# Kernel optimization log

Measured on AMD Instinct MI355X. Metric: run time of the kernel, lower is better.

Reference implementation:

```python
import jax, jax.numpy as jnp
import numpy as np

EMBED = 1024
D_MODEL = 1024
HEADS = 16
HEAD_DIM = D_MODEL // HEADS


def setup_inputs() -> dict:
    key = jax.random.key(0)
    ks = jax.random.split(key, 9)
    s = 1.0 / np.sqrt(EMBED)
    inp = {
        "x": jax.random.normal(ks[0], (4, 2048, EMBED), dtype=jnp.float32),
        "Wq": jax.random.uniform(ks[1], (EMBED, D_MODEL), jnp.float32, -s, s),
        "bq": jax.random.uniform(ks[2], (D_MODEL,), jnp.float32, -s, s),
        "Wk": jax.random.uniform(ks[3], (EMBED, D_MODEL), jnp.float32, -s, s),
        "bk": jax.random.uniform(ks[4], (D_MODEL,), jnp.float32, -s, s),
        "Wv": jax.random.uniform(ks[5], (EMBED, D_MODEL), jnp.float32, -s, s),
        "bv": jax.random.uniform(ks[6], (D_MODEL,), jnp.float32, -s, s),
        "Wo": jax.random.uniform(ks[7], (D_MODEL, D_MODEL), jnp.float32, -s, s),
        "bo": jax.random.uniform(ks[8], (D_MODEL,), jnp.float32, -s, s),
    }
    return inp


def reference(x, Wq, bq, Wk, bk, Wv, bv, Wo, bo):
    B, S, _ = x.shape
    # projections -> [B, H, S, Dh]
    def proj(W, b):
        return (x @ W + b).reshape(B, S, HEADS, HEAD_DIM).transpose(0, 2, 1, 3)
    q = proj(Wq, bq)
    k = proj(Wk, bk)
    v = proj(Wv, bv)
    energy = jnp.einsum("bhqd,bhkd->bhqk", q, k)  # [B,H,S,S]
    attn = jax.nn.softmax(energy / jnp.sqrt(jnp.float32(HEAD_DIM)), axis=-1)
    out = jnp.einsum("bhqk,bhkd->bhqd", attn, v)
    out = out.transpose(0, 2, 1, 3).reshape(B, S, D_MODEL)
    return out @ Wo + bo
```

## Files before the change

### kernel.cpp

```cpp
#include <hip/hip_runtime.h>

typedef unsigned short u16;
typedef unsigned int u32;
typedef unsigned short u16x8 __attribute__((ext_vector_type(8)));
typedef unsigned int u32x4 __attribute__((ext_vector_type(4)));
typedef __bf16 bf16x8 __attribute__((ext_vector_type(8)));
typedef float f32x4 __attribute__((ext_vector_type(4)));

#define QSCALE 0.18033688011112042f

__device__ __forceinline__ u16 f2bf(float f) {
    unsigned u = __float_as_uint(f);
    u += 0x7fffu + ((u >> 16) & 1u);
    return (u16)(u >> 16);
}

__device__ __forceinline__ u32 cvtpk(float lo, float hi) {
    u32 r;
    asm("v_cvt_pk_bf16_f32 %0, %1, %2" : "=v"(r) : "v"(lo), "v"(hi));
    return r;
}

__device__ __forceinline__ bf16x8 ldfrag(const u16* p) {
    return __builtin_bit_cast(bf16x8, *(const u16x8*)p);
}

__device__ __forceinline__ void async_cp16(const void* g, void* l) {
    __builtin_amdgcn_global_load_lds(
        (const __attribute__((address_space(1))) unsigned int*)g,
        (__attribute__((address_space(3))) unsigned int*)l, 16, 0, 0);
}

__device__ __forceinline__ uint2 pack4(float a, float b, float c, float d) {
    uint2 w;
    w.x = (u32)f2bf(a) | ((u32)f2bf(b) << 16);
    w.y = (u32)f2bf(c) | ((u32)f2bf(d) << 16);
    return w;
}

__device__ __forceinline__ f32x4 mfma32(bf16x8 a, bf16x8 b, f32x4 c) {
    return __builtin_amdgcn_mfma_f32_16x16x32_bf16(a, b, c, 0, 0, 0);
}


__global__ void cvt_x(const float* __restrict__ x, u16* __restrict__ xb, int n4) {
    int i = blockIdx.x * blockDim.x + threadIdx.x;
    if (i < n4) {
        float4 v = ((const float4*)x)[i];
        ushort4 o;
        o.x = f2bf(v.x); o.y = f2bf(v.y); o.z = f2bf(v.z); o.w = f2bf(v.w);
        ((ushort4*)xb)[i] = o;
    }
}

__global__ __launch_bounds__(1024) void transp(const float* __restrict__ src, u16* __restrict__ dst) {
    __shared__ float t[32][33];
    int bx = blockIdx.x * 32, by = blockIdx.y * 32;
    t[threadIdx.y][threadIdx.x] = src[(by + threadIdx.y) * 1024 + bx + threadIdx.x];
    __syncthreads();
    dst[(bx + threadIdx.y) * 1024 + by + threadIdx.x] = f2bf(t[threadIdx.x][threadIdx.y]);
}

__global__ void mkbias(const float* __restrict__ bq, const float* __restrict__ bk,
                       const float* __restrict__ bv, float* __restrict__ bqkv) {
    int i = blockIdx.x * blockDim.x + threadIdx.x;
    if (i < 3072) bqkv[i] = (i < 1024) ? bq[i] : (i < 2048 ? bk[i - 1024] : bv[i - 2048]);
}


template <int EPI>
__global__ __launch_bounds__(512)
void gemm256(const u16* __restrict__ A, const u16* __restrict__ Bt,
             const float* __restrict__ bias,
             u16* __restrict__ Qb, u16* __restrict__ Kb, u16* __restrict__ Vt,
             float* __restrict__ outf) {
    __shared__ u16 Asm3[3][256 * 64];
    __shared__ u16 Bsm3[3][128 * 64];

    int tid = threadIdx.x;
    int wave = tid >> 6, lane = tid & 63;
    int lr = lane & 15, lq = lane >> 4;
    int wrow = (wave >> 1) * 64, wcol = (wave & 1) * 64;
    int tileM = blockIdx.y * 256, tileN = blockIdx.x * 128;

    f32x4 acc[4][4];
#pragma unroll
    for (int i = 0; i < 4; i++)
#pragma unroll
        for (int j = 0; j < 4; j++)
            acc[i][j] = (f32x4){0.f, 0.f, 0.f, 0.f};

    int srow = tid >> 3;
    int sgrp = (tid & 7) ^ (srow & 7);
    const u16* gA = A + (tileM + srow) * 1024 + sgrp * 8;
    const u16* gB = Bt + (tileN + srow) * 1024 + sgrp * 8;

#define STAGE(buf, kc)                                                        \
    do {                                                                      \
        _Pragma("unroll")                                                     \
        for (int r = 0; r < 4; ++r)                                           \
            async_cp16(gA + (kc) + r * 64 * 1024, &Asm3[buf][tid * 8 + r * 4096]); \
        _Pragma("unroll")                                                     \
        for (int r = 0; r < 2; ++r)                                           \
            async_cp16(gB + (kc) + r * 64 * 1024, &Bsm3[buf][tid * 8 + r * 4096]); \
    } while (0)

    STAGE(0, 0);
    STAGE(1, 64);
    asm volatile("s_waitcnt vmcnt(6)" ::: "memory");
    __builtin_amdgcn_s_barrier();

    for (int t = 0; t < 16; ++t) {
        int cur = t % 3;
        STAGE((t + 2) % 3, ((t + 2) & 15) * 64);

        const u16* Ap = &Asm3[cur][0];
        const u16* Bp = &Bsm3[cur][0];
        bf16x8 af[4][2], bfr[2][2];
#pragma unroll
        for (int mt = 0; mt < 4; ++mt)
#pragma unroll
            for (int ko = 0; ko < 2; ++ko)
                af[mt][ko] = ldfrag(&Ap[(wrow + mt * 16 + lr) * 64 +
                                        (((ko * 4 + lq) ^ (lr & 7)) << 3)]);
#pragma unroll
        for (int nt = 0; nt < 2; ++nt)
#pragma unroll
            for (int ko = 0; ko < 2; ++ko)
                bfr[nt][ko] = ldfrag(&Bp[(wcol + nt * 16 + lr) * 64 +
                                         (((ko * 4 + lq) ^ (lr & 7)) << 3)]);
        bf16x8 bfr2[2][2];
#pragma unroll
        for (int nt = 0; nt < 2; ++nt)
#pragma unroll
            for (int ko = 0; ko < 2; ++ko)
                bfr2[nt][ko] = ldfrag(&Bp[(wcol + (nt + 2) * 16 + lr) * 64 +
                                          (((ko * 4 + lq) ^ (lr & 7)) << 3)]);

        asm volatile("s_waitcnt lgkmcnt(0)" ::: "memory");
        __builtin_amdgcn_sched_barrier(0);
        __builtin_amdgcn_s_setprio(1);
#pragma unroll
        for (int ko = 0; ko < 2; ++ko)
#pragma unroll
            for (int mt = 0; mt < 4; ++mt)
#pragma unroll
                for (int nt = 0; nt < 4; ++nt) {
                    bf16x8 b = (nt < 2) ? bfr[nt][ko] : bfr2[nt - 2][ko];
                    if (EPI == 1)
                        acc[mt][nt] = mfma32(af[mt][ko], b, acc[mt][nt]);
                    else
                        acc[mt][nt] = mfma32(b, af[mt][ko], acc[mt][nt]);
                }
        __builtin_amdgcn_s_setprio(0);
        asm volatile("s_waitcnt vmcnt(6)" ::: "memory");
        __builtin_amdgcn_s_barrier();
    }
    asm volatile("s_waitcnt vmcnt(0)" ::: "memory");
#undef STAGE

    if (EPI == 0) {
#pragma unroll
        for (int mt = 0; mt < 4; ++mt) {
            int m = tileM + wrow + mt * 16 + lr;
            int b = m >> 11, s = m & 2047;
#pragma unroll
            for (int nt = 0; nt < 4; ++nt) {
                int n0 = tileN + wcol + nt * 16 + lq * 4;
                float4 bn = *(const float4*)&bias[n0];
                int which = n0 >> 10, d = n0 & 1023, h = d >> 6, dh = d & 63;
                u16* dst = (which ? Kb : Qb) + ((b * 16 + h) * 2048 + s) * 64 + dh;
                f32x4 v = acc[mt][nt];
                uint2 w;
                if (which == 0)
                    w = pack4((v[0] + bn.x) * QSCALE, (v[1] + bn.y) * QSCALE,
                              (v[2] + bn.z) * QSCALE, (v[3] + bn.w) * QSCALE);
                else
                    w = pack4(v[0] + bn.x, v[1] + bn.y, v[2] + bn.z, v[3] + bn.w);
                *(uint2*)dst = w;
            }
        }
    } else if (EPI == 1) {
#pragma unroll
        for (int nt = 0; nt < 4; ++nt) {
            int n0 = tileN + wcol + nt * 16 + lr;
            float bn = bias[n0];
            int h = n0 >> 6, dh = n0 & 63;
#pragma unroll
            for (int mt = 0; mt < 4; ++mt) {
                int m0 = tileM + wrow + mt * 16 + lq * 4;
                int b = m0 >> 11, s = m0 & 2047;
                f32x4 v = acc[mt][nt];
                uint2 w = pack4(v[0] + bn, v[1] + bn, v[2] + bn, v[3] + bn);
                *(uint2*)(Vt + ((b * 16 + h) * 64 + dh) * 2048 + s) = w;
            }
        }
    } else {
#pragma unroll
        for (int mt = 0; mt < 4; ++mt) {
            int m = tileM + wrow + mt * 16 + lr;
#pragma unroll
            for (int nt = 0; nt < 4; ++nt) {
                int n0 = tileN + wcol + nt * 16 + lq * 4;
                float4 bn = *(const float4*)&bias[n0];
                f32x4 v = acc[mt][nt];
                float4 st = {v[0] + bn.x, v[1] + bn.y, v[2] + bn.z, v[3] + bn.w};
                *(float4*)&outf[m * 1024 + n0] = st;
            }
        }
    }
}

__global__ __launch_bounds__(256)
void attn(const u16* __restrict__ Qb, const u16* __restrict__ Kb,
          const u16* __restrict__ Vt, u16* __restrict__ Ob) {
    __shared__ u16 Ksm[2][64 * 64];
    __shared__ u16 Vsm[2][64 * 64];
    int tid = threadIdx.x;
    int wave = tid >> 6, lane = tid & 63;
    int lr = lane & 15, lq = lane >> 4;
    int bh = blockIdx.y;
    int b = bh >> 4, h = bh & 15;
    int qbase = blockIdx.x * 128 + wave * 32;

    const u16* Qh = Qb + bh * 2048 * 64;
    const u16* Kh = Kb + bh * 2048 * 64;
    const u16* Vh = Vt + bh * 64 * 2048;

    bf16x8 qf[2][2];
    for (int s = 0; s < 2; s++)
        for (int hf = 0; hf < 2; hf++)
            qf[s][hf] = ldfrag(Qh + (qbase + s * 16 + lr) * 64 + hf * 32 + lq * 8);

    f32x4 o[2][4];
    float lacc[2] = {0.f, 0.f};
    for (int s = 0; s < 2; s++)
        for (int dt = 0; dt < 4; dt++) o[s][dt] = (f32x4){0.f, 0.f, 0.f, 0.f};

    int row0 = ((lr & 12) << 1) | (lr & 3);
    int gg = (lr & 3) | (((lr >> 2) & 1) << 2);
    int kofs = row0 * 64 + ((lq ^ gg) << 3);
    int vofs0 = (lq ^ (lr & 7)) << 3;

    int sr = tid >> 3, sg = tid & 7;
    int gK = (sg ^ ((sr & 3) | (((sr >> 3) & 1) << 2))) << 3;
    int gV = (sg ^ (sr & 7)) << 3;
    const u16* gk = Kh + sr * 64 + gK;
    const u16* gv = Vh + sr * 2048 + gV;

    async_cp16(gk, &Ksm[0][tid * 8]);
    async_cp16(gk + 32 * 64, &Ksm[0][tid * 8 + 32 * 64]);
    async_cp16(gv, &Vsm[0][tid * 8]);
    async_cp16(gv + 32 * 2048, &Vsm[0][tid * 8 + 32 * 64]);

    for (int it = 0; it < 32; ++it) {
        int p = it & 1;
        __syncthreads();

        if (it < 31) {
            gk += 64 * 64; gv += 64;
            async_cp16(gk, &Ksm[p ^ 1][tid * 8]);
            async_cp16(gk + 32 * 64, &Ksm[p ^ 1][tid * 8 + 32 * 64]);
            async_cp16(gv, &Vsm[p ^ 1][tid * 8]);
            async_cp16(gv + 32 * 2048, &Vsm[p ^ 1][tid * 8 + 32 * 64]);
        }

        const u16* Kp = Ksm[p];
        const u16* Vp = Vsm[p];

        bf16x8 pb[2][2];
        for (int kg2 = 0; kg2 < 2; kg2++) {
            int ka = kofs + kg2 * 2048;
            bf16x8 kA0 = ldfrag(Kp + ka);
            bf16x8 kA1 = ldfrag(Kp + (ka ^ 32));
            bf16x8 kB0 = ldfrag(Kp + ka + 256);
            bf16x8 kB1 = ldfrag(Kp + ((ka + 256) ^ 32));
            for (int s = 0; s < 2; s++) {
                f32x4 sa = (f32x4){0.f, 0.f, 0.f, 0.f};
                f32x4 sb = (f32x4){0.f, 0.f, 0.f, 0.f};
                sa = mfma32(kA0, qf[s][0], sa);
                sa = mfma32(kA1, qf[s][1], sa);
                sb = mfma32(kB0, qf[s][0], sb);
                sb = mfma32(kB1, qf[s][1], sb);
                float e0 = __builtin_amdgcn_exp2f(sa[0]);
                float e1 = __builtin_amdgcn_exp2f(sa[1]);
                float e2 = __builtin_amdgcn_exp2f(sa[2]);
                float e3 = __builtin_amdgcn_exp2f(sa[3]);
                float e4 = __builtin_amdgcn_exp2f(sb[0]);
                float e5 = __builtin_amdgcn_exp2f(sb[1]);
                float e6 = __builtin_amdgcn_exp2f(sb[2]);
                float e7 = __builtin_amdgcn_exp2f(sb[3]);
                lacc[s] += ((e0 + e1) + (e2 + e3)) + ((e4 + e5) + (e6 + e7));
                u32x4 pw = {cvtpk(e0, e1), cvtpk(e2, e3), cvtpk(e4, e5), cvtpk(e6, e7)};
                pb[kg2][s] = __builtin_bit_cast(bf16x8, pw);
            }
        }

        for (int dt = 0; dt < 4; dt++) {
            int rb = (dt * 16 + lr) * 64;
            bf16x8 v0 = ldfrag(Vp + rb + vofs0);
            bf16x8 v1 = ldfrag(Vp + rb + (vofs0 ^ 32));
            o[0][dt] = mfma32(v0, pb[0][0], o[0][dt]);
            o[1][dt] = mfma32(v0, pb[0][1], o[1][dt]);
            o[0][dt] = mfma32(v1, pb[1][0], o[0][dt]);
            o[1][dt] = mfma32(v1, pb[1][1], o[1][dt]);
        }
    }

    for (int s = 0; s < 2; s++) {
        lacc[s] += __shfl_xor(lacc[s], 16);
        lacc[s] += __shfl_xor(lacc[s], 32);
    }

    for (int s = 0; s < 2; s++) {
        float linv = 1.0f / lacc[s];
        int q = qbase + s * 16 + lr;
        u16* obase = Ob + (b * 2048 + q) * 1024 + h * 64 + lq * 4;
        for (int dt = 0; dt < 4; dt++) {
            uint2 w = pack4(o[s][dt][0] * linv, o[s][dt][1] * linv,
                            o[s][dt][2] * linv, o[s][dt][3] * linv);
            *(uint2*)(obase + dt * 16) = w;
        }
    }
}


extern "C" void kernel_launch(void* const* d_in, const int* in_sizes, int n_in,
                              void* d_out, int out_size, void* d_ws, size_t ws_size,
                              hipStream_t stream) {
    const float* x  = (const float*)d_in[0];
    const float* Wq = (const float*)d_in[1];
    const float* bq = (const float*)d_in[2];
    const float* Wk = (const float*)d_in[3];
    const float* bk = (const float*)d_in[4];
    const float* Wv = (const float*)d_in[5];
    const float* bv = (const float*)d_in[6];
    const float* Wo = (const float*)d_in[7];
    const float* bo = (const float*)d_in[8];
    float* out = (float*)d_out;

    char* ws = (char*)d_ws;
    u16* xb    = (u16*)ws;
    u16* Wt    = (u16*)(ws + (16u << 20));
    u16* Wot   = (u16*)(ws + (22u << 20));
    float* bqkv = (float*)(ws + (24u << 20));
    u16* Vtb   = (u16*)(ws + (25u << 20));
    u16* Qb    = (u16*)d_out;
    u16* Kb    = Qb + 4 * 16 * 2048 * 64;

    cvt_x<<<8192, 256, 0, stream>>>(x, xb, 8192 * 1024 / 4);
    dim3 tb(32, 32);
    transp<<<dim3(32, 32), tb, 0, stream>>>(Wq, Wt);
    transp<<<dim3(32, 32), tb, 0, stream>>>(Wk, Wt + 1024 * 1024);
    transp<<<dim3(32, 32), tb, 0, stream>>>(Wv, Wt + 2 * 1024 * 1024);
    transp<<<dim3(32, 32), tb, 0, stream>>>(Wo, Wot);
    mkbias<<<12, 256, 0, stream>>>(bq, bk, bv, bqkv);

    gemm256<0><<<dim3(16, 32), 512, 0, stream>>>(xb, Wt, bqkv, Qb, Kb, nullptr, nullptr);
    gemm256<1><<<dim3(8, 32), 512, 0, stream>>>(xb, Wt + 2048 * 1024, bqkv + 2048,
                                                nullptr, nullptr, Vtb, nullptr);
    attn<<<dim3(16, 64), 256, 0, stream>>>(Qb, Kb, Vtb, xb);
    gemm256<2><<<dim3(8, 32), 512, 0, stream>>>(xb, Wot, bo, nullptr, nullptr, nullptr, out);
}
```

Before: 316.9 us.

## Restructure GEMM to 4 waves with 128x64 warp tiles and K=32 stages

Replaces the 512-thread GEMM with a 256-thread version where each wave computes a 128x64 sub-tile (8x4 MFMA tiles), doubling register accumulators per wave and improving fragment reuse per LDS read. K-chunk per stage halves to 32 with a new swizzle, shrinking LDS per block so two blocks can co-reside (launch_bounds 256,2). Trades more loop iterations and barriers and higher register pressure (128 accumulator floats) for better arithmetic intensity per wave and occupancy.

```diff
diff --git a/kernel.cpp b/kernel.cpp
--- a/kernel.cpp
+++ b/kernel.cpp
@@ -69,89 +69,75 @@
 
 
 template <int EPI>
-__global__ __launch_bounds__(512)
-void gemm256(const u16* __restrict__ A, const u16* __restrict__ Bt,
-             const float* __restrict__ bias,
-             u16* __restrict__ Qb, u16* __restrict__ Kb, u16* __restrict__ Vt,
-             float* __restrict__ outf) {
-    __shared__ u16 Asm3[3][256 * 64];
-    __shared__ u16 Bsm3[3][128 * 64];
+__global__ __launch_bounds__(256, 2)
+void gemmw(const u16* __restrict__ A, const u16* __restrict__ Bt,
+           const float* __restrict__ bias,
+           u16* __restrict__ Qb, u16* __restrict__ Kb, u16* __restrict__ Vt,
+           float* __restrict__ outf) {
+    __shared__ u16 Asm3[3][256 * 32];
+    __shared__ u16 Bsm3[3][128 * 32];
 
     int tid = threadIdx.x;
     int wave = tid >> 6, lane = tid & 63;
     int lr = lane & 15, lq = lane >> 4;
-    int wrow = (wave >> 1) * 64, wcol = (wave & 1) * 64;
+    int wrow = (wave >> 1) * 128, wcol = (wave & 1) * 64;
     int tileM = blockIdx.y * 256, tileN = blockIdx.x * 128;
 
-    f32x4 acc[4][4];
-#pragma unroll
-    for (int i = 0; i < 4; i++)
+    f32x4 acc[8][4];
+#pragma unroll
+    for (int i = 0; i < 8; i++)
 #pragma unroll
         for (int j = 0; j < 4; j++)
             acc[i][j] = (f32x4){0.f, 0.f, 0.f, 0.f};
 
-    int srow = tid >> 3;
-    int sgrp = (tid & 7) ^ (srow & 7);
+    int srow = tid >> 2;
+    int sgrp = (tid & 3) ^ (((tid >> 2) ^ (tid >> 4)) & 3);
     const u16* gA = A + (tileM + srow) * 1024 + sgrp * 8;
     const u16* gB = Bt + (tileN + srow) * 1024 + sgrp * 8;
 
-#define STAGE(buf, kc)                                                        \
-    do {                                                                      \
-        _Pragma("unroll")                                                     \
-        for (int r = 0; r < 4; ++r)                                           \
-            async_cp16(gA + (kc) + r * 64 * 1024, &Asm3[buf][tid * 8 + r * 4096]); \
-        _Pragma("unroll")                                                     \
-        for (int r = 0; r < 2; ++r)                                           \
-            async_cp16(gB + (kc) + r * 64 * 1024, &Bsm3[buf][tid * 8 + r * 4096]); \
+    int rofs = ((lq ^ ((lr ^ (lr >> 2)) & 3)) << 3);
+
+#define STAGE(buf, kc)                                                         \
+    do {                                                                       \
+        _Pragma("unroll")                                                      \
+        for (int r = 0; r < 4; ++r)                                            \
+            async_cp16(gA + (kc) + r * 64 * 1024, &Asm3[buf][tid * 8 + r * 2048]); \
+        _Pragma("unroll")                                                      \
+        for (int r = 0; r < 2; ++r)                                            \
+            async_cp16(gB + (kc) + r * 64 * 1024, &Bsm3[buf][tid * 8 + r * 2048]); \
     } while (0)
 
     STAGE(0, 0);
-    STAGE(1, 64);
+    STAGE(1, 32);
     asm volatile("s_waitcnt vmcnt(6)" ::: "memory");
     __builtin_amdgcn_s_barrier();
 
-    for (int t = 0; t < 16; ++t) {
+    for (int t = 0; t < 32; ++t) {
         int cur = t % 3;
-        STAGE((t + 2) % 3, ((t + 2) & 15) * 64);
+        STAGE((t + 2) % 3, ((t + 2) & 31) * 32);
 
         const u16* Ap = &Asm3[cur][0];
         const u16* Bp = &Bsm3[cur][0];
-        bf16x8 af[4][2], bfr[2][2];
-#pragma unroll
-        for (int mt = 0; mt < 4; ++mt)
-#pragma unroll
-            for (int ko = 0; ko < 2; ++ko)
-                af[mt][ko] = ldfrag(&Ap[(wrow + mt * 16 + lr) * 64 +
-                                        (((ko * 4 + lq) ^ (lr & 7)) << 3)]);
-#pragma unroll
-        for (int nt = 0; nt < 2; ++nt)
-#pragma unroll
-            for (int ko = 0; ko < 2; ++ko)
-                bfr[nt][ko] = ldfrag(&Bp[(wcol + nt * 16 + lr) * 64 +
-                                         (((ko * 4 + lq) ^ (lr & 7)) << 3)]);
-        bf16x8 bfr2[2][2];
-#pragma unroll
-        for (int nt = 0; nt < 2; ++nt)
-#pragma unroll
-            for (int ko = 0; ko < 2; ++ko)
-                bfr2[nt][ko] = ldfrag(&Bp[(wcol + (nt + 2) * 16 + lr) * 64 +
-                                          (((ko * 4 + lq) ^ (lr & 7)) << 3)]);
+        bf16x8 af[8], bf[4];
+#pragma unroll
+        for (int mt = 0; mt < 8; ++mt)
+            af[mt] = ldfrag(&Ap[(wrow + mt * 16 + lr) * 32 + rofs]);
+#pragma unroll
+        for (int nt = 0; nt < 4; ++nt)
+            bf[nt] = ldfrag(&Bp[(wcol + nt * 16 + lr) * 32 + rofs]);
 
         asm volatile("s_waitcnt lgkmcnt(0)" ::: "memory");
         __builtin_amdgcn_sched_barrier(0);
         __builtin_amdgcn_s_setprio(1);
 #pragma unroll
-        for (int ko = 0; ko < 2; ++ko)
-#pragma unroll
-            for (int mt = 0; mt < 4; ++mt)
-#pragma unroll
-                for (int nt = 0; nt < 4; ++nt) {
-                    bf16x8 b = (nt < 2) ? bfr[nt][ko] : bfr2[nt - 2][ko];
-                    if (EPI == 1)
-                        acc[mt][nt] = mfma32(af[mt][ko], b, acc[mt][nt]);
-                    else
-                        acc[mt][nt] = mfma32(b, af[mt][ko], acc[mt][nt]);
-                }
+        for (int mt = 0; mt < 8; ++mt)
+#pragma unroll
+            for (int nt = 0; nt < 4; ++nt) {
+                if (EPI == 1)
+                    acc[mt][nt] = mfma32(af[mt], bf[nt], acc[mt][nt]);
+                else
+                    acc[mt][nt] = mfma32(bf[nt], af[mt], acc[mt][nt]);
+            }
         __builtin_amdgcn_s_setprio(0);
         asm volatile("s_waitcnt vmcnt(6)" ::: "memory");
         __builtin_amdgcn_s_barrier();
@@ -161,7 +147,7 @@
 
     if (EPI == 0) {
 #pragma unroll
-        for (int mt = 0; mt < 4; ++mt) {
+        for (int mt = 0; mt < 8; ++mt) {
             int m = tileM + wrow + mt * 16 + lr;
             int b = m >> 11, s = m & 2047;
 #pragma unroll
@@ -187,7 +173,7 @@
             float bn = bias[n0];
             int h = n0 >> 6, dh = n0 & 63;
 #pragma unroll
-            for (int mt = 0; mt < 4; ++mt) {
+            for (int mt = 0; mt < 8; ++mt) {
                 int m0 = tileM + wrow + mt * 16 + lq * 4;
                 int b = m0 >> 11, s = m0 & 2047;
                 f32x4 v = acc[mt][nt];
@@ -197,7 +183,7 @@
         }
     } else {
 #pragma unroll
-        for (int mt = 0; mt < 4; ++mt) {
+        for (int mt = 0; mt < 8; ++mt) {
             int m = tileM + wrow + mt * 16 + lr;
 #pragma unroll
             for (int nt = 0; nt < 4; ++nt) {
@@ -356,9 +342,9 @@
     transp<<<dim3(32, 32), tb, 0, stream>>>(Wo, Wot);
     mkbias<<<12, 256, 0, stream>>>(bq, bk, bv, bqkv);
 
-    gemm256<0><<<dim3(16, 32), 512, 0, stream>>>(xb, Wt, bqkv, Qb, Kb, nullptr, nullptr);
-    gemm256<1><<<dim3(8, 32), 512, 0, stream>>>(xb, Wt + 2048 * 1024, bqkv + 2048,
-                                                nullptr, nullptr, Vtb, nullptr);
+    gemmw<0><<<dim3(16, 32), 256, 0, stream>>>(xb, Wt, bqkv, Qb, Kb, nullptr, nullptr);
+    gemmw<1><<<dim3(8, 32), 256, 0, stream>>>(xb, Wt + 2048 * 1024, bqkv + 2048,
+                                              nullptr, nullptr, Vtb, nullptr);
     attn<<<dim3(16, 64), 256, 0, stream>>>(Qb, Kb, Vtb, xb);
-    gemm256<2><<<dim3(8, 32), 512, 0, stream>>>(xb, Wot, bo, nullptr, nullptr, nullptr, out);
-}
+    gemmw<2><<<dim3(8, 32), 256, 0, stream>>>(xb, Wot, bo, nullptr, nullptr, nullptr, out);
+}
```

Result: slower. 336.5 us (+6.2%).
